# Kernel tuning notes

Measured on AMD Instinct MI355X. Metric: run time of the kernel, lower is better.

Reference implementation:

```python
import jax, jax.numpy as jnp
import numpy as np


def setup_inputs() -> dict:
    key = jax.random.key(0)
    k1, k2, k3 = jax.random.split(key, 3)
    batch, h, num_logical, n_pairs = 2048, 128, 64, 512
    # P: (batch, h, h) soft assignment (approximately doubly stochastic via row softmax)
    P = jax.nn.softmax(jax.random.uniform(k1, (batch, h, h), dtype=jnp.float32) * 4.0, axis=-1)
    # d_error: (h, h) precomputed nonnegative error-distance matrix, symmetric w/ zero diag
    d = jax.random.uniform(k2, (h, h), dtype=jnp.float32)
    d_error = (d + d.T) * (1.0 - jnp.eye(h, dtype=jnp.float32))
    circuit_edge_pairs = jax.random.randint(k3, (n_pairs, 2), 0, num_logical, dtype=jnp.int64)
    return {"P": P, "d_error": d_error, "circuit_edge_pairs": circuit_edge_pairs, "num_logical": num_logical}


def reference(P, d_error, circuit_edge_pairs, num_logical):
    # Restrict to logical-qubit rows, then gather both endpoints of every circuit edge.
    P_logical = P[:, :num_logical, :]                      # (b, L, h)
    P_i = P_logical[:, circuit_edge_pairs[:, 0], :]        # (b, E, h)
    P_j = P_logical[:, circuit_edge_pairs[:, 1], :]        # (b, E, h)
    # cost[b,e] = sum_{p,q} P_i[b,e,p] * d_error[p,q] * P_j[b,e,q]
    cost = jnp.einsum('bep,pq,beq->be', P_i, d_error, P_j)
    # sum_e mean_b(cost) / E == mean over (b, e)
    return jnp.mean(cost)
```

## Files before the change

### kernel.cpp

```cpp
#include <hip/hip_runtime.h>
#include <hip/hip_bf16.h>

#define B_TOTAL 2048
#define H 128
#define NL 64
#define NPAIRS 512
#define BPB 2
#define K1_BLOCKS (B_TOTAL / BPB)
#define AT_STRIDE 72
#define S_STRIDE 72

typedef __attribute__((ext_vector_type(8))) short bf16x8;
typedef __attribute__((ext_vector_type(4))) float f32x4;

static __device__ __forceinline__ ushort f2bf(float f) {
    uint u = __float_as_uint(f);
    u += 0x7fffu + ((u >> 16) & 1u);
    return (ushort)(u >> 16);
}

__global__ void build_S_kernel(const int* __restrict__ pairs,
                               ushort* __restrict__ S_bf) {
    __shared__ int cnt[NL * NL];
    const int tid = threadIdx.x;
    for (int k = tid; k < NL * NL; k += 256) cnt[k] = 0;
    __syncthreads();
    for (int e = tid; e < NPAIRS; e += 256) {
        int i = pairs[2 * e] & (NL - 1);
        int j = pairs[2 * e + 1] & (NL - 1);
        atomicAdd(&cnt[i * NL + j], 1);
    }
    __syncthreads();
    for (int k = tid; k < NL * S_STRIDE; k += 256) {
        int r = k / S_STRIDE, c = k - r * S_STRIDE;
        float v = (c < NL) ? (float)cnt[r * NL + c] : 0.0f;
        S_bf[k] = f2bf(v);
    }
}

__global__ __launch_bounds__(256, 2)
void edge_loss_mfma(const float* __restrict__ P,
                    const float* __restrict__ D,
                    const ushort* __restrict__ S_ws,
                    float* __restrict__ out) {
    __shared__ float  As[NL][H];
    __shared__ ushort ATb[H][AT_STRIDE];
    __shared__ ushort YTb[H][AT_STRIDE];
    __shared__ ushort Sb[NL][S_STRIDE];
    __shared__ float  wsum[4];

    const int tid  = threadIdx.x;
    const int lane = tid & 63;
    const int w    = tid >> 6;
    const int l15  = lane & 15;
    const int lg   = lane >> 4;

    {
        const uint* src = reinterpret_cast<const uint*>(S_ws);
        uint* dst = reinterpret_cast<uint*>(&Sb[0][0]);
        for (int k = tid; k < NL * S_STRIDE / 2; k += 256) dst[k] = src[k];
    }

    f32x4 acc[8][2];
#pragma unroll
    for (int a = 0; a < 8; ++a) {
        acc[a][0] = (f32x4)0.0f;
        acc[a][1] = (f32x4)0.0f;
    }

    for (int bb = 0; bb < BPB; ++bb) {
        const int b = blockIdx.x * BPB + bb;

        {
            const float4* src = reinterpret_cast<const float4*>(P + (size_t)b * H * H);
            float4* dst = reinterpret_cast<float4*>(&As[0][0]);
#pragma unroll
            for (int k = 0; k < 8; ++k) dst[tid + k * 256] = src[tid + k * 256];
        }
        __syncthreads();

        {
            const int q  = tid >> 1;
            const int i0 = (tid & 1) * 32;
#pragma unroll
            for (int g = 0; g < 4; ++g) {
                const int ib = i0 + g * 8;
                uint4 v;
                v.x = (uint)f2bf(As[ib + 0][q]) | ((uint)f2bf(As[ib + 1][q]) << 16);
                v.y = (uint)f2bf(As[ib + 2][q]) | ((uint)f2bf(As[ib + 3][q]) << 16);
                v.z = (uint)f2bf(As[ib + 4][q]) | ((uint)f2bf(As[ib + 5][q]) << 16);
                v.w = (uint)f2bf(As[ib + 6][q]) | ((uint)f2bf(As[ib + 7][q]) << 16);
                *reinterpret_cast<uint4*>(&ATb[q][ib]) = v;
            }
        }
        __syncthreads();

        {
            f32x4 yt[2][4];
#pragma unroll
            for (int m = 0; m < 2; ++m)
#pragma unroll
                for (int nt = 0; nt < 4; ++nt) yt[m][nt] = (f32x4)0.0f;

#pragma unroll
            for (int ks = 0; ks < 2; ++ks) {
                const int kcol = ks * 32 + lg * 8;
                bf16x8 a0 = *reinterpret_cast<const bf16x8*>(&ATb[(2 * w + 0) * 16 + l15][kcol]);
                bf16x8 a1 = *reinterpret_cast<const bf16x8*>(&ATb[(2 * w + 1) * 16 + l15][kcol]);
#pragma unroll
                for (int nt = 0; nt < 4; ++nt) {
                    bf16x8 sf = *reinterpret_cast<const bf16x8*>(&Sb[nt * 16 + l15][kcol]);
                    yt[0][nt] = __builtin_amdgcn_mfma_f32_16x16x32_bf16(a0, sf, yt[0][nt], 0, 0, 0);
                    yt[1][nt] = __builtin_amdgcn_mfma_f32_16x16x32_bf16(a1, sf, yt[1][nt], 0, 0, 0);
                }
            }
#pragma unroll
            for (int m = 0; m < 2; ++m)
#pragma unroll
                for (int nt = 0; nt < 4; ++nt)
#pragma unroll
                    for (int r = 0; r < 4; ++r) {
                        const int qrow = (2 * w + m) * 16 + lg * 4 + r;
                        YTb[qrow][nt * 16 + l15] = f2bf(yt[m][nt][r]);
                    }
        }

#pragma unroll
        for (int ks = 0; ks < 2; ++ks) {
            const int kcol = ks * 32 + lg * 8;
            bf16x8 b0 = *reinterpret_cast<const bf16x8*>(&YTb[(2 * w + 0) * 16 + l15][kcol]);
            bf16x8 b1 = *reinterpret_cast<const bf16x8*>(&YTb[(2 * w + 1) * 16 + l15][kcol]);
#pragma unroll
            for (int pt = 0; pt < 8; ++pt) {
                bf16x8 af = *reinterpret_cast<const bf16x8*>(&ATb[pt * 16 + l15][kcol]);
                acc[pt][0] = __builtin_amdgcn_mfma_f32_16x16x32_bf16(af, b0, acc[pt][0], 0, 0, 0);
                acc[pt][1] = __builtin_amdgcn_mfma_f32_16x16x32_bf16(af, b1, acc[pt][1], 0, 0, 0);
            }
        }
        __syncthreads();
    }

    float s = 0.0f;
#pragma unroll
    for (int pt = 0; pt < 8; ++pt) {
#pragma unroll
        for (int nq = 0; nq < 2; ++nq) {
            const int col  = (2 * w + nq) * 16 + l15;
            const int row0 = pt * 16 + lg * 4;
#pragma unroll
            for (int r = 0; r < 4; ++r)
                s = fmaf(acc[pt][nq][r], D[(size_t)(row0 + r) * H + col], s);
        }
    }
#pragma unroll
    for (int off = 32; off > 0; off >>= 1) s += __shfl_down(s, off, 64);

    if (lane == 0) wsum[w] = s;
    __syncthreads();
    if (tid == 0) {
        float t = wsum[0] + wsum[1] + wsum[2] + wsum[3];
        atomicAdd(out, t * (1.0f / ((float)B_TOTAL * (float)NPAIRS)));
    }
}

extern "C" void kernel_launch(void* const* d_in, const int* in_sizes, int n_in,
                              void* d_out, int out_size, void* d_ws, size_t ws_size,
                              hipStream_t stream) {
    const float* P     = (const float*)d_in[0];
    const float* D     = (const float*)d_in[1];
    const int*   pairs = (const int*)d_in[2];
    float* out = (float*)d_out;

    ushort* S_bf = (ushort*)d_ws;

    hipMemsetAsync(d_out, 0, sizeof(float), stream);
    build_S_kernel<<<1, 256, 0, stream>>>(pairs, S_bf);
    edge_loss_mfma<<<K1_BLOCKS, 256, 0, stream>>>(P, D, S_bf, out);
}
```

Baseline: 197.3 us.

## Reassociate edge loss as (P D Pᵀ)·S with swizzled bf16 LDS and prefetch

The contraction order changes. Instead of computing Pᵀ S P and dotting it with D, each block now computes U = P_L·D (64x128 by 128x128), then M = U·P_Lᵀ, and dots M with the pair-count matrix S held in registers. D is converted to bf16 once in a widened prep kernel and stored in LDS with an XOR swizzle, replacing the transposed, padded layout. The next batch's P rows are prefetched into registers and converted to bf16 during compute, with double-buffered LDS so only one barrier per batch remains. This removes the fp32 staging and transpose pass, but roughly doubles the first GEMM's K dimension and adds more LDS traffic for D.

```diff
diff --git a/kernel.cpp b/kernel.cpp
--- a/kernel.cpp
+++ b/kernel.cpp
@@ -6,9 +6,7 @@
 #define NL 64
 #define NPAIRS 512
 #define BPB 2
-#define K1_BLOCKS (B_TOTAL / BPB)
-#define AT_STRIDE 72
-#define S_STRIDE 72
+#define NBLOCKS (B_TOTAL / BPB)
 
 typedef __attribute__((ext_vector_type(8))) short bf16x8;
 typedef __attribute__((ext_vector_type(4))) float f32x4;
@@ -18,162 +16,165 @@
     u += 0x7fffu + ((u >> 16) & 1u);
     return (ushort)(u >> 16);
 }
+static __device__ __forceinline__ uint pk2bf(float x, float y) {
+    return (uint)f2bf(x) | ((uint)f2bf(y) << 16);
+}
 
-__global__ void build_S_kernel(const int* __restrict__ pairs,
-                               ushort* __restrict__ S_bf) {
-    __shared__ int cnt[NL * NL];
+__global__ void prep_kernel(const int* __restrict__ pairs,
+                            const float* __restrict__ Dsrc,
+                            float* __restrict__ Sf,
+                            ushort* __restrict__ Dbf) {
     const int tid = threadIdx.x;
-    for (int k = tid; k < NL * NL; k += 256) cnt[k] = 0;
-    __syncthreads();
-    for (int e = tid; e < NPAIRS; e += 256) {
-        int i = pairs[2 * e] & (NL - 1);
-        int j = pairs[2 * e + 1] & (NL - 1);
-        atomicAdd(&cnt[i * NL + j], 1);
-    }
-    __syncthreads();
-    for (int k = tid; k < NL * S_STRIDE; k += 256) {
-        int r = k / S_STRIDE, c = k - r * S_STRIDE;
-        float v = (c < NL) ? (float)cnt[r * NL + c] : 0.0f;
-        S_bf[k] = f2bf(v);
+    if (blockIdx.x == 0) {
+        __shared__ int cnt[NL * NL];
+        for (int k = tid; k < NL * NL; k += 256) cnt[k] = 0;
+        __syncthreads();
+        for (int e = tid; e < NPAIRS; e += 256) {
+            int i = pairs[2 * e] & (NL - 1);
+            int j = pairs[2 * e + 1] & (NL - 1);
+            atomicAdd(&cnt[i * NL + j], 1);
+        }
+        __syncthreads();
+        for (int k = tid; k < NL * NL; k += 256) Sf[k] = (float)cnt[k];
+    } else {
+        int k = (blockIdx.x - 1) * 256 + tid;
+        Dbf[k] = f2bf(Dsrc[k]);
     }
 }
 
 __global__ __launch_bounds__(256, 2)
-void edge_loss_mfma(const float* __restrict__ P,
-                    const float* __restrict__ D,
-                    const ushort* __restrict__ S_ws,
-                    float* __restrict__ out) {
-    __shared__ float  As[NL][H];
-    __shared__ ushort ATb[H][AT_STRIDE];
-    __shared__ ushort YTb[H][AT_STRIDE];
-    __shared__ ushort Sb[NL][S_STRIDE];
-    __shared__ float  wsum[4];
+void edge_loss_v3(const float* __restrict__ P,
+                  const float* __restrict__ Sf,
+                  const ushort* __restrict__ Dbf,
+                  float* __restrict__ out) {
+    __shared__ ushort lds[40960];
+    ushort* Db  = lds;
+    ushort* Ab0 = lds + 16384;
+    ushort* Ab1 = lds + 16384 + 8192;
+    ushort* Ub  = lds + 16384 + 16384;
 
     const int tid  = threadIdx.x;
     const int lane = tid & 63;
     const int w    = tid >> 6;
     const int l15  = lane & 15;
     const int lg   = lane >> 4;
+    const uint rmask = (uint)(l15 & 7) << 4;
+    const int rowa = 16 * w + l15;
 
     {
-        const uint* src = reinterpret_cast<const uint*>(S_ws);
-        uint* dst = reinterpret_cast<uint*>(&Sb[0][0]);
-        for (int k = tid; k < NL * S_STRIDE / 2; k += 256) dst[k] = src[k];
+        const uint4* src = reinterpret_cast<const uint4*>(Dbf);
+        for (int k = tid; k < 2048; k += 256) {
+            int row = k >> 4, gc = k & 15;
+            int gs = gc ^ (row & 7);
+            *reinterpret_cast<uint4*>((char*)Db + row * 256 + gs * 16) = src[k];
+        }
     }
 
-    f32x4 acc[8][2];
+    float sreg[4][4];
 #pragma unroll
-    for (int a = 0; a < 8; ++a) {
-        acc[a][0] = (f32x4)0.0f;
-        acc[a][1] = (f32x4)0.0f;
-    }
+    for (int nt = 0; nt < 4; ++nt)
+#pragma unroll
+        for (int r = 0; r < 4; ++r)
+            sreg[nt][r] = Sf[(16 * w + 4 * lg + r) * NL + nt * 16 + l15];
+
+    f32x4 m[4];
+#pragma unroll
+    for (int nt = 0; nt < 4; ++nt) m[nt] = (f32x4)0.0f;
+
+    float4 pf[8];
+    const int b0 = blockIdx.x * BPB;
+    auto loadA = [&](int b) {
+        const float4* src = reinterpret_cast<const float4*>(P + (size_t)b * H * H);
+#pragma unroll
+        for (int k = 0; k < 8; ++k) pf[k] = src[tid + k * 256];
+    };
+    auto cvtStore = [&](ushort* dst) {
+#pragma unroll
+        for (int k = 0; k < 8; ++k) {
+            int f4 = tid + k * 256;
+            int i  = f4 >> 5;
+            int q4 = (f4 & 31) * 4;
+            uint2 d2;
+            d2.x = pk2bf(pf[k].x, pf[k].y);
+            d2.y = pk2bf(pf[k].z, pf[k].w);
+            *reinterpret_cast<uint2*>((char*)dst + i * 256 + ((q4 * 2) ^ ((i & 7) << 4))) = d2;
+        }
+    };
+
+    loadA(b0);
+    cvtStore(Ab0);
+    __syncthreads();
 
     for (int bb = 0; bb < BPB; ++bb) {
-        const int b = blockIdx.x * BPB + bb;
+        const ushort* A_ = (bb & 1) ? Ab1 : Ab0;
+        if (bb + 1 < BPB) loadA(b0 + bb + 1);
 
-        {
-            const float4* src = reinterpret_cast<const float4*>(P + (size_t)b * H * H);
-            float4* dst = reinterpret_cast<float4*>(&As[0][0]);
+        f32x4 u[8];
 #pragma unroll
-            for (int k = 0; k < 8; ++k) dst[tid + k * 256] = src[tid + k * 256];
-        }
-        __syncthreads();
-
-        {
-            const int q  = tid >> 1;
-            const int i0 = (tid & 1) * 32;
+        for (int nt = 0; nt < 8; ++nt) u[nt] = (f32x4)0.0f;
 #pragma unroll
-            for (int g = 0; g < 4; ++g) {
-                const int ib = i0 + g * 8;
-                uint4 v;
-                v.x = (uint)f2bf(As[ib + 0][q]) | ((uint)f2bf(As[ib + 1][q]) << 16);
-                v.y = (uint)f2bf(As[ib + 2][q]) | ((uint)f2bf(As[ib + 3][q]) << 16);
-                v.z = (uint)f2bf(As[ib + 4][q]) | ((uint)f2bf(As[ib + 5][q]) << 16);
-                v.w = (uint)f2bf(As[ib + 6][q]) | ((uint)f2bf(As[ib + 7][q]) << 16);
-                *reinterpret_cast<uint4*>(&ATb[q][ib]) = v;
+        for (int ks = 0; ks < 4; ++ks) {
+            const uint koff = (uint)(ks * 64 + lg * 16);
+            bf16x8 a = *reinterpret_cast<const bf16x8*>((const char*)A_ + rowa * 256 + (koff ^ rmask));
+#pragma unroll
+            for (int nt = 0; nt < 8; ++nt) {
+                bf16x8 d = *reinterpret_cast<const bf16x8*>((const char*)Db + (nt * 16 + l15) * 256 + (koff ^ rmask));
+                u[nt] = __builtin_amdgcn_mfma_f32_16x16x32_bf16(a, d, u[nt], 0, 0, 0);
             }
         }
-        __syncthreads();
-
-        {
-            f32x4 yt[2][4];
 #pragma unroll
-            for (int m = 0; m < 2; ++m)
+        for (int nt = 0; nt < 8; ++nt)
 #pragma unroll
-                for (int nt = 0; nt < 4; ++nt) yt[m][nt] = (f32x4)0.0f;
-
-#pragma unroll
-            for (int ks = 0; ks < 2; ++ks) {
-                const int kcol = ks * 32 + lg * 8;
-                bf16x8 a0 = *reinterpret_cast<const bf16x8*>(&ATb[(2 * w + 0) * 16 + l15][kcol]);
-                bf16x8 a1 = *reinterpret_cast<const bf16x8*>(&ATb[(2 * w + 1) * 16 + l15][kcol]);
-#pragma unroll
-                for (int nt = 0; nt < 4; ++nt) {
-                    bf16x8 sf = *reinterpret_cast<const bf16x8*>(&Sb[nt * 16 + l15][kcol]);
-                    yt[0][nt] = __builtin_amdgcn_mfma_f32_16x16x32_bf16(a0, sf, yt[0][nt], 0, 0, 0);
-                    yt[1][nt] = __builtin_amdgcn_mfma_f32_16x16x32_bf16(a1, sf, yt[1][nt], 0, 0, 0);
-                }
+            for (int r = 0; r < 4; ++r) {
+                int row = 16 * w + 4 * lg + r;
+                *reinterpret_cast<ushort*>((char*)Ub + row * 256 +
+                    (((uint)((nt * 16 + l15) * 2)) ^ ((uint)(row & 7) << 4))) = f2bf(u[nt][r]);
             }
 #pragma unroll
-            for (int m = 0; m < 2; ++m)
+        for (int ks = 0; ks < 4; ++ks) {
+            const uint koff = (uint)(ks * 64 + lg * 16);
+            bf16x8 a2 = *reinterpret_cast<const bf16x8*>((const char*)Ub + rowa * 256 + (koff ^ rmask));
 #pragma unroll
-                for (int nt = 0; nt < 4; ++nt)
-#pragma unroll
-                    for (int r = 0; r < 4; ++r) {
-                        const int qrow = (2 * w + m) * 16 + lg * 4 + r;
-                        YTb[qrow][nt * 16 + l15] = f2bf(yt[m][nt][r]);
-                    }
-        }
-
-#pragma unroll
-        for (int ks = 0; ks < 2; ++ks) {
-            const int kcol = ks * 32 + lg * 8;
-            bf16x8 b0 = *reinterpret_cast<const bf16x8*>(&YTb[(2 * w + 0) * 16 + l15][kcol]);
-            bf16x8 b1 = *reinterpret_cast<const bf16x8*>(&YTb[(2 * w + 1) * 16 + l15][kcol]);
-#pragma unroll
-            for (int pt = 0; pt < 8; ++pt) {
-                bf16x8 af = *reinterpret_cast<const bf16x8*>(&ATb[pt * 16 + l15][kcol]);
-                acc[pt][0] = __builtin_amdgcn_mfma_f32_16x16x32_bf16(af, b0, acc[pt][0], 0, 0, 0);
-                acc[pt][1] = __builtin_amdgcn_mfma_f32_16x16x32_bf16(af, b1, acc[pt][1], 0, 0, 0);
+            for (int nt = 0; nt < 4; ++nt) {
+                bf16x8 bf = *reinterpret_cast<const bf16x8*>((const char*)A_ + (nt * 16 + l15) * 256 + (koff ^ rmask));
+                m[nt] = __builtin_amdgcn_mfma_f32_16x16x32_bf16(a2, bf, m[nt], 0, 0, 0);
             }
         }
-        __syncthreads();
+        if (bb + 1 < BPB) {
+            cvtStore((bb & 1) ? Ab0 : Ab1);
+            __syncthreads();
+        }
     }
 
     float s = 0.0f;
 #pragma unroll
-    for (int pt = 0; pt < 8; ++pt) {
+    for (int nt = 0; nt < 4; ++nt)
 #pragma unroll
-        for (int nq = 0; nq < 2; ++nq) {
-            const int col  = (2 * w + nq) * 16 + l15;
-            const int row0 = pt * 16 + lg * 4;
-#pragma unroll
-            for (int r = 0; r < 4; ++r)
-                s = fmaf(acc[pt][nq][r], D[(size_t)(row0 + r) * H + col], s);
-        }
-    }
+        for (int r = 0; r < 4; ++r) s = fmaf(m[nt][r], sreg[nt][r], s);
 #pragma unroll
     for (int off = 32; off > 0; off >>= 1) s += __shfl_down(s, off, 64);
 
+    __syncthreads();
+    float* wsum = reinterpret_cast<float*>(Db);
     if (lane == 0) wsum[w] = s;
     __syncthreads();
-    if (tid == 0) {
-        float t = wsum[0] + wsum[1] + wsum[2] + wsum[3];
-        atomicAdd(out, t * (1.0f / ((float)B_TOTAL * (float)NPAIRS)));
-    }
+    if (tid == 0)
+        atomicAdd(out, (wsum[0] + wsum[1] + wsum[2] + wsum[3]) *
+                       (1.0f / ((float)B_TOTAL * (float)NPAIRS)));
 }
 
 extern "C" void kernel_launch(void* const* d_in, const int* in_sizes, int n_in,
                               void* d_out, int out_size, void* d_ws, size_t ws_size,
                               hipStream_t stream) {
     const float* P     = (const float*)d_in[0];
-    const float* D     = (const float*)d_in[1];
+    const float* Dsrc  = (const float*)d_in[1];
     const int*   pairs = (const int*)d_in[2];
     float* out = (float*)d_out;
 
-    ushort* S_bf = (ushort*)d_ws;
+    float*  Sf  = (float*)d_ws;
+    ushort* Dbf = (ushort*)((char*)d_ws + NL * NL * 4);
 
     hipMemsetAsync(d_out, 0, sizeof(float), stream);
-    build_S_kernel<<<1, 256, 0, stream>>>(pairs, S_bf);
-    edge_loss_mfma<<<K1_BLOCKS, 256, 0, stream>>>(P, D, S_bf, out);
+    prep_kernel<<<65, 256, 0, stream>>>(pairs, Dsrc, Sf, Dbf);
+    edge_loss_v3<<<NBLOCKS, 256, 0, stream>>>(P, Sf, Dbf, out);
 }
```

New measurement: 192.6 us. 1.02x faster.
